# Performance work log

Measured on AMD Instinct MI355X. Metric: run time of the kernel, lower is better.

The kernel has to match this reference:

```python
import jax, jax.numpy as jnp
import numpy as np

USER_COUNT = 100000
ITEM_COUNT = 50000
N_NODES = USER_COUNT + ITEM_COUNT
EMB = 64
N_EDGES = 1250000
BATCH = 4096
GCN_LAYERS = 3


def setup_inputs() -> dict:
    key = jax.random.key(0)
    k = jax.random.split(key, 7)
    return {
        "user_emb": jax.random.normal(k[0], (USER_COUNT, EMB), dtype=jnp.float32) * 0.1,
        "item_emb": jax.random.normal(k[1], (ITEM_COUNT, EMB), dtype=jnp.float32) * 0.1,
        "edge_row": jax.random.randint(k[2], (N_EDGES,), 0, N_NODES, dtype=jnp.int32),
        "edge_col": jax.random.randint(k[3], (N_EDGES,), 0, N_NODES, dtype=jnp.int32),
        "edge_weight": jax.random.uniform(k[4], (N_EDGES,), dtype=jnp.float32) * 0.1,
        "users": jax.random.randint(k[5], (BATCH,), 0, USER_COUNT, dtype=jnp.int32),
        "items": jax.random.randint(k[6], (BATCH,), 0, ITEM_COUNT, dtype=jnp.int32),
    }


def reference(user_emb, item_emb, edge_row, edge_col, edge_weight, users, items):
    # ego = cat(user_emb, item_emb) : [N, d]
    ego = jnp.concatenate([user_emb, item_emb], axis=0)
    n = ego.shape[0]
    acc = ego  # running sum of hop embeddings (mean taken at the end)
    x = ego
    for _ in range(GCN_LAYERS):
        # SpMM: out[r] += w_e * x[c] for each edge e=(r,c)
        x = jax.ops.segment_sum(edge_weight[:, None] * x[edge_col], edge_row,
                                num_segments=n)
        acc = acc + x
    all_emb = acc / jnp.float32(GCN_LAYERS + 1)  # mean over stacked hops
    user_all = all_emb[:user_emb.shape[0]]
    item_all = all_emb[user_emb.shape[0]:]
    return (user_all[users], item_all[items])
```

## Files before the change

kernel.cpp:

```cpp
#include <hip/hip_runtime.h>

#define USER_COUNT 100000
#define ITEM_COUNT 50000
#define N_NODES    150000
#define EMB        64
#define N_EDGES    1250000
#define BATCH      4096

#define BROWS     512
#define NBKT      293
#define A1_TILE   2048
#define A1_BLOCKS ((N_EDGES + A1_TILE - 1) / A1_TILE)
#define PSTR      320
#define COLMASK   0x3FFFFu
#define ROW_ALLOC 150536
#define CSR_CAP   5120

#define CONCAT_BLOCKS 9375

static __device__ __forceinline__ unsigned pack_bf16x2(float a, float b) {
    unsigned ua = __float_as_uint(a);
    unsigned ub = __float_as_uint(b);
    ua += 0x7FFFu + ((ua >> 16) & 1u);
    ub += 0x7FFFu + ((ub >> 16) & 1u);
    return (ua >> 16) | (ub & 0xFFFF0000u);
}

static __device__ __forceinline__ const float* ego_ptr(unsigned c,
                                                       const float* __restrict__ ue,
                                                       const float* __restrict__ ie) {
    return (c < USER_COUNT) ? ue + (size_t)c * EMB
                            : ie + (size_t)(c - USER_COUNT) * EMB;
}

static __device__ __forceinline__ void fma4(float4& a, float w, uint2 p) {
    a.x += w * __uint_as_float(p.x << 16);
    a.y += w * __uint_as_float(p.x & 0xFFFF0000u);
    a.z += w * __uint_as_float(p.y << 16);
    a.w += w * __uint_as_float(p.y & 0xFFFF0000u);
}

static __device__ __forceinline__ float4 spmm_row16(const uint2* __restrict__ edges,
                                                    int s, int e,
                                                    const uint2* __restrict__ x2,
                                                    int l) {
    float4 a0 = {0.f,0.f,0.f,0.f}, a1 = {0.f,0.f,0.f,0.f};
    float4 a2 = {0.f,0.f,0.f,0.f}, a3 = {0.f,0.f,0.f,0.f};
    int i = s;
    for (; i + 7 < e; i += 8) {
        uint2 e0 = edges[i],     e1 = edges[i + 1];
        uint2 e2 = edges[i + 2], e3 = edges[i + 3];
        uint2 e4 = edges[i + 4], e5 = edges[i + 5];
        uint2 e6 = edges[i + 6], e7 = edges[i + 7];
        uint2 p0 = x2[(size_t)(e0.x & COLMASK) * 16 + l];
        uint2 p1 = x2[(size_t)(e1.x & COLMASK) * 16 + l];
        uint2 p2 = x2[(size_t)(e2.x & COLMASK) * 16 + l];
        uint2 p3 = x2[(size_t)(e3.x & COLMASK) * 16 + l];
        uint2 p4 = x2[(size_t)(e4.x & COLMASK) * 16 + l];
        uint2 p5 = x2[(size_t)(e5.x & COLMASK) * 16 + l];
        uint2 p6 = x2[(size_t)(e6.x & COLMASK) * 16 + l];
        uint2 p7 = x2[(size_t)(e7.x & COLMASK) * 16 + l];
        fma4(a0, __uint_as_float(e0.y), p0);
        fma4(a1, __uint_as_float(e1.y), p1);
        fma4(a2, __uint_as_float(e2.y), p2);
        fma4(a3, __uint_as_float(e3.y), p3);
        fma4(a0, __uint_as_float(e4.y), p4);
        fma4(a1, __uint_as_float(e5.y), p5);
        fma4(a2, __uint_as_float(e6.y), p6);
        fma4(a3, __uint_as_float(e7.y), p7);
    }
    if (i + 3 < e) {
        uint2 e0 = edges[i],     e1 = edges[i + 1];
        uint2 e2 = edges[i + 2], e3 = edges[i + 3];
        uint2 p0 = x2[(size_t)(e0.x & COLMASK) * 16 + l];
        uint2 p1 = x2[(size_t)(e1.x & COLMASK) * 16 + l];
        uint2 p2 = x2[(size_t)(e2.x & COLMASK) * 16 + l];
        uint2 p3 = x2[(size_t)(e3.x & COLMASK) * 16 + l];
        fma4(a0, __uint_as_float(e0.y), p0);
        fma4(a1, __uint_as_float(e1.y), p1);
        fma4(a2, __uint_as_float(e2.y), p2);
        fma4(a3, __uint_as_float(e3.y), p3);
        i += 4;
    }
    for (; i < e; ++i) {
        uint2 e0 = edges[i];
        uint2 p0 = x2[(size_t)(e0.x & COLMASK) * 16 + l];
        fma4(a0, __uint_as_float(e0.y), p0);
    }
    float4 r;
    r.x = (a0.x + a1.x) + (a2.x + a3.x);
    r.y = (a0.y + a1.y) + (a2.y + a3.y);
    r.z = (a0.z + a1.z) + (a2.z + a3.z);
    r.w = (a0.w + a1.w) + (a2.w + a3.w);
    return r;
}

__global__ void k_hist(const int* __restrict__ row, int* __restrict__ partT) {
    __shared__ int h[PSTR];
    int tid = threadIdx.x;
    int bb  = blockIdx.x;
    h[tid] = 0;
    if (tid + 256 < PSTR) h[tid + 256] = 0;
    __syncthreads();
    int base = bb * A1_TILE;
    #pragma unroll
    for (int j = 0; j < 8; ++j) {
        int e = base + j * 256 + tid;
        if (e < N_EDGES) atomicAdd(&h[row[e] >> 9], 1);
    }
    __syncthreads();
    if (tid < NBKT) partT[bb * PSTR + tid] = h[tid];
    if (tid + 256 < NBKT) partT[bb * PSTR + tid + 256] = h[tid + 256];
}

__global__ void k_scanbkt(int* __restrict__ partT, int* __restrict__ gtot) {
    __shared__ int sA[256], sB[256];
    int t   = blockIdx.x;
    int tid = threadIdx.x;
    int v0 = 0, v1 = 0, v2 = 0;
    int b0 = tid * 3;
    if (b0 + 0 < A1_BLOCKS) v0 = partT[(b0 + 0) * PSTR + t];
    if (b0 + 1 < A1_BLOCKS) v1 = partT[(b0 + 1) * PSTR + t];
    if (b0 + 2 < A1_BLOCKS) v2 = partT[(b0 + 2) * PSTR + t];
    int s = v0 + v1 + v2;
    sA[tid] = s;
    __syncthreads();
    int* in = sA; int* out = sB;
    for (int off = 1; off < 256; off <<= 1) {
        out[tid] = in[tid] + ((tid >= off) ? in[tid - off] : 0);
        __syncthreads();
        int* tmp = in; in = out; out = tmp;
    }
    int run = in[tid] - s;
    if (b0 + 0 < A1_BLOCKS) { partT[(b0 + 0) * PSTR + t] = run; run += v0; }
    if (b0 + 1 < A1_BLOCKS) { partT[(b0 + 1) * PSTR + t] = run; run += v1; }
    if (b0 + 2 < A1_BLOCKS) { partT[(b0 + 2) * PSTR + t] = run; }
    if (tid == 255) gtot[t] = in[255];
}

__global__ void k_binfill_concat(const int* __restrict__ row,
                                 const int* __restrict__ col,
                                 const float* __restrict__ w,
                                 const int* __restrict__ partT,
                                 const int* __restrict__ gtot,
                                 uint2* __restrict__ edges_a,
                                 const float* __restrict__ ue,
                                 const float* __restrict__ ie,
                                 unsigned* __restrict__ x) {
    __shared__ int cnt[512], cnt2[PSTR], gpos[PSTR], sc[PSTR];
    __shared__ int sA[512], sB[512];
    __shared__ uint2 srec[A1_TILE];
    __shared__ int  sdst[A1_TILE];
    int tid = threadIdx.x;

    if (blockIdx.x >= A1_BLOCKS) {
        const size_t nu4 = (size_t)USER_COUNT * EMB / 4;
        size_t i = (size_t)(blockIdx.x - A1_BLOCKS) * 256 + tid;
        float4 v = (i < nu4) ? ((const float4*)ue)[i] : ((const float4*)ie)[i - nu4];
        uint2 p;
        p.x = pack_bf16x2(v.x, v.y);
        p.y = pack_bf16x2(v.z, v.w);
        ((uint2*)x)[i] = p;
        return;
    }

    cnt[tid] = 0; cnt[tid + 256] = 0;
    cnt2[tid] = 0;
    if (tid + 256 < PSTR) cnt2[tid + 256] = 0;
    __syncthreads();

    int ebase   = blockIdx.x * A1_TILE;
    int tilecnt = min(A1_TILE, N_EDGES - ebase);

    int r[8], c[8]; float wv[8];
    #pragma unroll
    for (int j = 0; j < 8; ++j) {
        int e = ebase + j * 256 + tid;
        if (e < N_EDGES) {
            r[j] = row[e]; c[j] = col[e]; wv[j] = w[e];
            atomicAdd(&cnt[r[j] >> 9], 1);
        } else {
            r[j] = -1;
        }
    }
    __syncthreads();

    {
        int ga = (tid < NBKT) ? gtot[tid] : 0;
        int gb = (tid + 256 < NBKT) ? gtot[tid + 256] : 0;
        int* in = sA; int* out = sB;
        in[tid] = ga; in[tid + 256] = gb;
        __syncthreads();
        for (int off = 1; off < 512; off <<= 1) {
            out[tid] = in[tid] + ((tid >= off) ? in[tid - off] : 0);
            int i2 = tid + 256;
            out[i2] = in[i2] + ((i2 >= off) ? in[i2 - off] : 0);
            __syncthreads();
            int* t = in; in = out; out = t;
        }
        gpos[tid] = in[tid] - ga;
        if (tid + 256 < PSTR) gpos[tid + 256] = in[tid + 256] - gb;
    }
    __syncthreads();

    {
        int* in = sA; int* out = sB;
        in[tid] = cnt[tid]; in[tid + 256] = cnt[tid + 256];
        __syncthreads();
        for (int off = 1; off < 512; off <<= 1) {
            out[tid] = in[tid] + ((tid >= off) ? in[tid - off] : 0);
            int i2 = tid + 256;
            out[i2] = in[i2] + ((i2 >= off) ? in[i2 - off] : 0);
            __syncthreads();
            int* t = in; in = out; out = t;
        }
        #pragma unroll
        for (int k = 0; k < 2; ++k) {
            int b = tid + k * 256;
            if (b < NBKT) {
                sc[b]    = in[b] - cnt[b];
                gpos[b] += partT[blockIdx.x * PSTR + b];
            }
        }
    }
    __syncthreads();

    #pragma unroll
    for (int j = 0; j < 8; ++j) {
        if (r[j] >= 0) {
            int b  = r[j] >> 9;
            int lp = sc[b] + atomicAdd(&cnt2[b], 1);
            srec[lp] = make_uint2((unsigned)c[j] | ((unsigned)(r[j] & 511) << 18),
                                  __float_as_uint(wv[j]));
            sdst[lp] = gpos[b] + (lp - sc[b]);
        }
    }
    __syncthreads();

    #pragma unroll
    for (int j = 0; j < 8; ++j) {
        int i = j * 256 + tid;
        if (i < tilecnt) edges_a[sdst[i]] = srec[i];
    }
}

__global__ __launch_bounds__(512) void k_csrfill(const int* __restrict__ gtot,
                                                 const uint2* __restrict__ edges_a,
                                                 uint2* __restrict__ edges_b,
                                                 int* __restrict__ row_start) {
    __shared__ uint2 srec[CSR_CAP];
    __shared__ int hist[256], cur[256];
    __shared__ int sA[512], sB[512];
    __shared__ int sbase, s_c0;
    int tid = threadIdx.x;
    int b   = blockIdx.x >> 1;
    int h   = blockIdx.x & 1;

    {
        int ga = (tid < NBKT) ? gtot[tid] : 0;
        int* in = sA; int* out = sB;
        in[tid] = ga;
        if (tid < 256) { int gb = (tid + 256 < NBKT) ? gtot[tid + 256] : 0;
                         in[tid + 256] = gb; }
        __syncthreads();
        for (int off = 1; off < 512; off <<= 1) {
            out[tid] = in[tid] + ((tid >= off) ? in[tid - off] : 0);
            __syncthreads();
            int* t = in; in = out; out = t;
        }
        if (tid == 0) { sbase = (b == 0) ? 0 : in[b - 1]; s_c0 = 0; }
        __syncthreads();
    }
    int base  = sbase;
    int count = gtot[b];

    if (tid < 256) { hist[tid] = 0; }
    __syncthreads();

    int c0 = 0;
    for (int i = tid; i < count; i += 512) {
        uint2 rec = edges_a[base + i];
        if (i < CSR_CAP) srec[i] = rec;
        int rl = (rec.x >> 18) & 511;
        c0 += (rl < 256);
        if ((rl >> 8) == h) atomicAdd(&hist[rl & 255], 1);
    }
    if (c0) atomicAdd(&s_c0, c0);
    __syncthreads();

    int halfbase = base + (h ? s_c0 : 0);

    {
        int hv = (tid < 256) ? hist[tid] : 0;
        int* in = sA; int* out = sB;
        if (tid < 256) in[tid] = hv;
        __syncthreads();
        for (int off = 1; off < 256; off <<= 1) {
            if (tid < 256) out[tid] = in[tid] + ((tid >= off) ? in[tid - off] : 0);
            __syncthreads();
            int* t = in; in = out; out = t;
        }
        if (tid < 256) {
            int excl = in[tid] - hv;
            row_start[b * BROWS + h * 256 + tid] = halfbase + excl;
            cur[tid] = halfbase + excl;
        }
    }
    __syncthreads();

    for (int i = tid; i < count; i += 512) {
        uint2 rec = (i < CSR_CAP) ? srec[i] : edges_a[base + i];
        int rl = (rec.x >> 18) & 511;
        if ((rl >> 8) != h) continue;
        int pos = atomicAdd(&cur[rl & 255], 1);
        edges_b[pos] = rec;
    }
}

__global__ void k_spmm_bf16(const int* __restrict__ row_start,
                            const uint2* __restrict__ edges,
                            const uint2* __restrict__ xin2,
                            uint2* __restrict__ xout2) {
    int g = blockIdx.x * 16 + (threadIdx.x >> 4);
    int l = threadIdx.x & 15;
    if (g >= N_NODES) return;
    float4 a = spmm_row16(edges, row_start[g], row_start[g + 1], xin2, l);
    xout2[(size_t)g * 16 + l] = make_uint2(pack_bf16x2(a.x, a.y),
                                           pack_bf16x2(a.z, a.w));
}

__global__ void k_epilogue(const int* __restrict__ users,
                           const int* __restrict__ items,
                           const float* __restrict__ ue,
                           const float* __restrict__ ie,
                           const uint2* __restrict__ x1,
                           const uint2* __restrict__ x2,
                           const int* __restrict__ row_start,
                           const uint2* __restrict__ edges,
                           float* __restrict__ out) {
    int g = blockIdx.x * 16 + (threadIdx.x >> 4);
    int l = threadIdx.x & 15;
    if (g >= 2 * BATCH) return;
    int node = (g < BATCH) ? users[g] : USER_COUNT + items[g - BATCH];
    float4 l3 = spmm_row16(edges, row_start[node], row_start[node + 1], x2, l);
    float4 e = ((const float4*)ego_ptr((unsigned)node, ue, ie))[l];
    uint2 pa = x1[(size_t)node * 16 + l];
    uint2 pb = x2[(size_t)node * 16 + l];
    float4 r;
    r.x = 0.25f * (e.x + __uint_as_float(pa.x << 16)
                       + __uint_as_float(pb.x << 16)         + l3.x);
    r.y = 0.25f * (e.y + __uint_as_float(pa.x & 0xFFFF0000u)
                       + __uint_as_float(pb.x & 0xFFFF0000u) + l3.y);
    r.z = 0.25f * (e.z + __uint_as_float(pa.y << 16)
                       + __uint_as_float(pb.y << 16)         + l3.z);
    r.w = 0.25f * (e.w + __uint_as_float(pa.y & 0xFFFF0000u)
                       + __uint_as_float(pb.y & 0xFFFF0000u) + l3.w);
    ((float4*)out)[(size_t)g * 16 + l] = r;
}

extern "C" void kernel_launch(void* const* d_in, const int* in_sizes, int n_in,
                              void* d_out, int out_size, void* d_ws, size_t ws_size,
                              hipStream_t stream) {
    const float* user_emb    = (const float*)d_in[0];
    const float* item_emb    = (const float*)d_in[1];
    const int*   edge_row    = (const int*)d_in[2];
    const int*   edge_col    = (const int*)d_in[3];
    const float* edge_weight = (const float*)d_in[4];
    const int*   users       = (const int*)d_in[5];
    const int*   items       = (const int*)d_in[6];
    float* out = (float*)d_out;

    const size_t node_u32 = (size_t)N_NODES * 32;
    unsigned* xa        = (unsigned*)d_ws;
    unsigned* xb        = xa + node_u32;
    unsigned* xc        = xb + node_u32;
    int*      row_start = (int*)(xc + node_u32);
    int*      gtot      = row_start + ROW_ALLOC;
    int*      partT     = gtot + 512;
    uint2*    edges_a   = (uint2*)(partT + A1_BLOCKS * PSTR);
    uint2*    edges_b   = edges_a + N_EDGES;

    k_hist<<<A1_BLOCKS, 256, 0, stream>>>(edge_row, partT);
    k_scanbkt<<<NBKT, 256, 0, stream>>>(partT, gtot);
    k_binfill_concat<<<A1_BLOCKS + CONCAT_BLOCKS, 256, 0, stream>>>(
        edge_row, edge_col, edge_weight, partT, gtot, edges_a,
        user_emb, item_emb, xa);
    k_csrfill<<<NBKT * 2, 512, 0, stream>>>(gtot, edges_a, edges_b, row_start);
    k_spmm_bf16<<<(N_NODES + 15) / 16, 256, 0, stream>>>(row_start, edges_b,
                                                         (const uint2*)xa,
                                                         (uint2*)xb);
    k_spmm_bf16<<<(N_NODES + 15) / 16, 256, 0, stream>>>(row_start, edges_b,
                                                         (const uint2*)xb,
                                                         (uint2*)xc);
    k_epilogue<<<(2 * BATCH + 15) / 16, 256, 0, stream>>>(users, items,
                                                          user_emb, item_emb,
                                                          (const uint2*)xb,
                                                          (const uint2*)xc,
                                                          row_start, edges_b,
                                                          out);
}
```

Before: 122.0 us.

## Compute second-hop SpMM only for rows reachable from the batch nodes

The epilogue needs layer 3 only for the 8192 batch nodes, and layer 2 only at those nodes and their neighbours. Extra blocks in the first SpMM kernel gather the batch nodes and their CSR neighbours into a global list. The second SpMM then runs only over that list instead of all 150k rows. This removes most of the second full SpMM pass, at the cost of atomics, possible duplicate rows in the list, and an unordered list that weakens locality.

```diff
diff --git a/kernel.cpp b/kernel.cpp
--- a/kernel.cpp
+++ b/kernel.cpp
@@ -17,6 +17,10 @@
 #define CSR_CAP   5120
 
 #define CONCAT_BLOCKS 9375
+#define SPMM_BLOCKS   9375
+#define MARK_BLOCKS   512
+#define LIST_BLOCKS   5000
+#define NLIST_CAP     524288
 
 static __device__ __forceinline__ unsigned pack_bf16x2(float a, float b) {
     unsigned ua = __float_as_uint(a);
@@ -113,10 +117,12 @@
     if (tid + 256 < NBKT) partT[bb * PSTR + tid + 256] = h[tid + 256];
 }
 
-__global__ void k_scanbkt(int* __restrict__ partT, int* __restrict__ gtot) {
+__global__ void k_scanbkt(int* __restrict__ partT, int* __restrict__ gtot,
+                          int* __restrict__ ncount) {
     __shared__ int sA[256], sB[256];
     int t   = blockIdx.x;
     int tid = threadIdx.x;
+    if (t == 0 && tid == 0) ncount[0] = 0;
     int v0 = 0, v1 = 0, v2 = 0;
     int b0 = tid * 3;
     if (b0 + 0 < A1_BLOCKS) v0 = partT[(b0 + 0) * PSTR + t];
@@ -317,16 +323,63 @@
     }
 }
 
-__global__ void k_spmm_bf16(const int* __restrict__ row_start,
+__global__ void k_spmm1_mark(const int* __restrict__ row_start,
+                             const uint2* __restrict__ edges,
+                             const uint2* __restrict__ xin2,
+                             uint2* __restrict__ xout2,
+                             const int* __restrict__ users,
+                             const int* __restrict__ items,
+                             int* __restrict__ nlist, int* __restrict__ ncount) {
+    __shared__ int lbuf[2048];
+    __shared__ int lcnt, gbase;
+    int tid = threadIdx.x;
+    if (blockIdx.x < SPMM_BLOCKS) {
+        int g = blockIdx.x * 16 + (tid >> 4);
+        int l = tid & 15;
+        if (g >= N_NODES) return;
+        float4 a = spmm_row16(edges, row_start[g], row_start[g + 1], xin2, l);
+        xout2[(size_t)g * 16 + l] = make_uint2(pack_bf16x2(a.x, a.y),
+                                               pack_bf16x2(a.z, a.w));
+    } else {
+        if (tid == 0) lcnt = 0;
+        __syncthreads();
+        int g = (blockIdx.x - SPMM_BLOCKS) * 16 + (tid >> 4);
+        int l = tid & 15;
+        if (g < 2 * BATCH) {
+            int node = (g < BATCH) ? users[g] : USER_COUNT + items[g - BATCH];
+            if (l == 0) {
+                int p = atomicAdd(&lcnt, 1);
+                if (p < 2048) lbuf[p] = node;
+            }
+            int s = row_start[node], e = row_start[node + 1];
+            for (int i = s + l; i < e; i += 16) {
+                int p = atomicAdd(&lcnt, 1);
+                if (p < 2048) lbuf[p] = (int)(edges[i].x & COLMASK);
+            }
+        }
+        __syncthreads();
+        int n = min(lcnt, 2048);
+        if (tid == 0) gbase = atomicAdd(ncount, n);
+        __syncthreads();
+        for (int i = tid; i < n; i += 256) nlist[gbase + i] = lbuf[i];
+    }
+}
+
+__global__ void k_spmm_list(const int* __restrict__ row_start,
                             const uint2* __restrict__ edges,
                             const uint2* __restrict__ xin2,
-                            uint2* __restrict__ xout2) {
-    int g = blockIdx.x * 16 + (threadIdx.x >> 4);
-    int l = threadIdx.x & 15;
-    if (g >= N_NODES) return;
-    float4 a = spmm_row16(edges, row_start[g], row_start[g + 1], xin2, l);
-    xout2[(size_t)g * 16 + l] = make_uint2(pack_bf16x2(a.x, a.y),
-                                           pack_bf16x2(a.z, a.w));
+                            uint2* __restrict__ xout2,
+                            const int* __restrict__ list,
+                            const int* __restrict__ count) {
+    int l   = threadIdx.x & 15;
+    int cnt = *count;
+    int ng  = gridDim.x * 16;
+    for (int gi = blockIdx.x * 16 + (threadIdx.x >> 4); gi < cnt; gi += ng) {
+        int g = list[gi];
+        float4 a = spmm_row16(edges, row_start[g], row_start[g + 1], xin2, l);
+        xout2[(size_t)g * 16 + l] = make_uint2(pack_bf16x2(a.x, a.y),
+                                               pack_bf16x2(a.z, a.w));
+    }
 }
 
 __global__ void k_epilogue(const int* __restrict__ users,
@@ -376,22 +429,24 @@
     unsigned* xc        = xb + node_u32;
     int*      row_start = (int*)(xc + node_u32);
     int*      gtot      = row_start + ROW_ALLOC;
-    int*      partT     = gtot + 512;
+    int*      ncount    = gtot + 512;
+    int*      nlist     = ncount + 16;
+    int*      partT     = nlist + NLIST_CAP;
     uint2*    edges_a   = (uint2*)(partT + A1_BLOCKS * PSTR);
     uint2*    edges_b   = edges_a + N_EDGES;
 
     k_hist<<<A1_BLOCKS, 256, 0, stream>>>(edge_row, partT);
-    k_scanbkt<<<NBKT, 256, 0, stream>>>(partT, gtot);
+    k_scanbkt<<<NBKT, 256, 0, stream>>>(partT, gtot, ncount);
     k_binfill_concat<<<A1_BLOCKS + CONCAT_BLOCKS, 256, 0, stream>>>(
         edge_row, edge_col, edge_weight, partT, gtot, edges_a,
         user_emb, item_emb, xa);
     k_csrfill<<<NBKT * 2, 512, 0, stream>>>(gtot, edges_a, edges_b, row_start);
-    k_spmm_bf16<<<(N_NODES + 15) / 16, 256, 0, stream>>>(row_start, edges_b,
-                                                         (const uint2*)xa,
-                                                         (uint2*)xb);
-    k_spmm_bf16<<<(N_NODES + 15) / 16, 256, 0, stream>>>(row_start, edges_b,
-                                                         (const uint2*)xb,
-                                                         (uint2*)xc);
+    k_spmm1_mark<<<SPMM_BLOCKS + MARK_BLOCKS, 256, 0, stream>>>(
+        row_start, edges_b, (const uint2*)xa, (uint2*)xb,
+        users, items, nlist, ncount);
+    k_spmm_list<<<LIST_BLOCKS, 256, 0, stream>>>(row_start, edges_b,
+                                                 (const uint2*)xb, (uint2*)xc,
+                                                 nlist, ncount);
     k_epilogue<<<(2 * BATCH + 15) / 16, 256, 0, stream>>>(users, items,
                                                           user_emb, item_emb,
                                                           (const uint2*)xb,
```

Measured after the change: 114.2 us, median of 2. 1.07x faster.

## Compute second and third hops only for batch nodes in the epilogue

Applied to the files above, without the earlier changes.

Drops the full-graph second SpMM pass. The epilogue now computes layer 2 for the requested node and layer 3 by walking its neighbours and running a row SpMM for each one over layer 1. This avoids propagating layer 2 across all 150k nodes, since only 8192 output rows are needed. The cost is redundant two-hop gather work per batch node (about 8 neighbours times 8 edges) and extra latency within each wave, but total traffic should be much lower than a full pass.

```diff
diff --git a/kernel.cpp b/kernel.cpp
--- a/kernel.cpp
+++ b/kernel.cpp
@@ -17,6 +17,7 @@
 #define CSR_CAP   5120
 
 #define CONCAT_BLOCKS 9375
+#define SPMM_BLOCKS   9375
 
 static __device__ __forceinline__ unsigned pack_bf16x2(float a, float b) {
     unsigned ua = __float_as_uint(a);
@@ -329,33 +330,50 @@
                                            pack_bf16x2(a.z, a.w));
 }
 
-__global__ void k_epilogue(const int* __restrict__ users,
-                           const int* __restrict__ items,
-                           const float* __restrict__ ue,
-                           const float* __restrict__ ie,
-                           const uint2* __restrict__ x1,
-                           const uint2* __restrict__ x2,
-                           const int* __restrict__ row_start,
-                           const uint2* __restrict__ edges,
-                           float* __restrict__ out) {
-    int g = blockIdx.x * 16 + (threadIdx.x >> 4);
-    int l = threadIdx.x & 15;
+__global__ void k_epilogue2(const int* __restrict__ users,
+                            const int* __restrict__ items,
+                            const float* __restrict__ ue,
+                            const float* __restrict__ ie,
+                            const uint2* __restrict__ x1,
+                            const int* __restrict__ row_start,
+                            const uint2* __restrict__ edges,
+                            float* __restrict__ out) {
+    int g = blockIdx.x * 8 + (threadIdx.x >> 5);
     if (g >= 2 * BATCH) return;
+    int lane = threadIdx.x & 31;
+    int h = lane >> 4;
+    int l = lane & 15;
     int node = (g < BATCH) ? users[g] : USER_COUNT + items[g - BATCH];
-    float4 l3 = spmm_row16(edges, row_start[node], row_start[node + 1], x2, l);
-    float4 e = ((const float4*)ego_ptr((unsigned)node, ue, ie))[l];
-    uint2 pa = x1[(size_t)node * 16 + l];
-    uint2 pb = x2[(size_t)node * 16 + l];
-    float4 r;
-    r.x = 0.25f * (e.x + __uint_as_float(pa.x << 16)
-                       + __uint_as_float(pb.x << 16)         + l3.x);
-    r.y = 0.25f * (e.y + __uint_as_float(pa.x & 0xFFFF0000u)
-                       + __uint_as_float(pb.x & 0xFFFF0000u) + l3.y);
-    r.z = 0.25f * (e.z + __uint_as_float(pa.y << 16)
-                       + __uint_as_float(pb.y << 16)         + l3.z);
-    r.w = 0.25f * (e.w + __uint_as_float(pa.y & 0xFFFF0000u)
-                       + __uint_as_float(pb.y & 0xFFFF0000u) + l3.w);
-    ((float4*)out)[(size_t)g * 16 + l] = r;
+    int s = row_start[node], e = row_start[node + 1];
+
+    float4 tot = {0.f, 0.f, 0.f, 0.f};
+    if (h == 0)
+        tot = spmm_row16(edges, s, e, x1, l);
+
+    for (int i = s + h; i < e; i += 2) {
+        uint2 rec = edges[i];
+        int   c   = (int)(rec.x & COLMASK);
+        float w   = __uint_as_float(rec.y);
+        float4 r  = spmm_row16(edges, row_start[c], row_start[c + 1], x1, l);
+        tot.x += w * r.x; tot.y += w * r.y;
+        tot.z += w * r.z; tot.w += w * r.w;
+    }
+
+    tot.x += __shfl_xor(tot.x, 16);
+    tot.y += __shfl_xor(tot.y, 16);
+    tot.z += __shfl_xor(tot.z, 16);
+    tot.w += __shfl_xor(tot.w, 16);
+
+    if (h == 0) {
+        float4 eg = ((const float4*)ego_ptr((unsigned)node, ue, ie))[l];
+        uint2  pa = x1[(size_t)node * 16 + l];
+        float4 r;
+        r.x = 0.25f * (eg.x + __uint_as_float(pa.x << 16)         + tot.x);
+        r.y = 0.25f * (eg.y + __uint_as_float(pa.x & 0xFFFF0000u) + tot.y);
+        r.z = 0.25f * (eg.z + __uint_as_float(pa.y << 16)         + tot.z);
+        r.w = 0.25f * (eg.w + __uint_as_float(pa.y & 0xFFFF0000u) + tot.w);
+        ((float4*)out)[(size_t)g * 16 + l] = r;
+    }
 }
 
 extern "C" void kernel_launch(void* const* d_in, const int* in_sizes, int n_in,
@@ -373,8 +391,7 @@
     const size_t node_u32 = (size_t)N_NODES * 32;
     unsigned* xa        = (unsigned*)d_ws;
     unsigned* xb        = xa + node_u32;
-    unsigned* xc        = xb + node_u32;
-    int*      row_start = (int*)(xc + node_u32);
+    int*      row_start = (int*)(xb + node_u32);
     int*      gtot      = row_start + ROW_ALLOC;
     int*      partT     = gtot + 512;
     uint2*    edges_a   = (uint2*)(partT + A1_BLOCKS * PSTR);
@@ -386,16 +403,11 @@
         edge_row, edge_col, edge_weight, partT, gtot, edges_a,
         user_emb, item_emb, xa);
     k_csrfill<<<NBKT * 2, 512, 0, stream>>>(gtot, edges_a, edges_b, row_start);
-    k_spmm_bf16<<<(N_NODES + 15) / 16, 256, 0, stream>>>(row_start, edges_b,
-                                                         (const uint2*)xa,
-                                                         (uint2*)xb);
-    k_spmm_bf16<<<(N_NODES + 15) / 16, 256, 0, stream>>>(row_start, edges_b,
+    k_spmm_bf16<<<SPMM_BLOCKS, 256, 0, stream>>>(row_start, edges_b,
+                                                 (const uint2*)xa, (uint2*)xb);
+    k_epilogue2<<<(2 * BATCH + 7) / 8, 256, 0, stream>>>(users, items,
+                                                         user_emb, item_emb,
                                                          (const uint2*)xb,
-                                                         (uint2*)xc);
-    k_epilogue<<<(2 * BATCH + 15) / 16, 256, 0, stream>>>(users, items,
-                                                          user_emb, item_emb,
-                                                          (const uint2*)xb,
-                                                          (const uint2*)xc,
-                                                          row_start, edges_b,
-                                                          out);
-}
+                                                         row_start, edges_b,
+                                                         out);
+}
```

Result: no change. 121.6 us (-0.3%).
